# Optimization experiments

Hardware: AMD Instinct MI355X
Metric: run time of the kernel (lower is better)

## Reference

```python
import jax, jax.numpy as jnp
import numpy as np

N_NODES = 100000
N_EDGES = 1600000
D_FEAT = 64
D_OUT = 64


def setup_inputs() -> dict:
    key = jax.random.key(0)
    k1, k2, k3, k4 = jax.random.split(key, 4)
    vertices = jax.random.normal(k1, (N_NODES, D_FEAT), dtype=jnp.float32)
    edges = jax.random.randint(k2, (2, N_EDGES), 0, N_NODES, dtype=jnp.int64)
    weight = jax.random.normal(k3, (D_OUT, D_FEAT), dtype=jnp.float32) * (1.0 / np.sqrt(D_FEAT))
    bias = jax.random.normal(k4, (D_OUT,), dtype=jnp.float32) * 0.01
    return {"vertices": vertices, "edges": edges, "weight": weight, "bias": bias}


def reference(vertices, edges, weight, bias):
    # GraphConv forward, dense (non-sparse) path, self_loop=True, normalize=True.
    n_vertices = vertices.shape[0]
    idx = jnp.arange(n_vertices, dtype=edges.dtype)
    dst = jnp.concatenate([edges[0], idx])  # scatter destinations (edges[0])
    src = jnp.concatenate([edges[1], idx])  # gather sources (edges[1])
    # agg[i] = sum over edges with dst==i of vertices[src]
    agg = jax.ops.segment_sum(vertices[src], dst, num_segments=n_vertices)
    # degree per node (torch scatters ones_like(neighbours): all feature cols equal)
    deg = jax.ops.segment_sum(
        jnp.ones_like(dst, dtype=vertices.dtype), dst, num_segments=n_vertices
    )
    agg = agg * (jnp.clip(deg, 1.0, None) ** -0.5)[:, None]
    # Linear: y = agg @ W.T + b
    return agg @ weight.T + bias
```

## Files before the change

kernel.cpp:

```cpp
#include <hip/hip_runtime.h>
#include <hip/hip_fp16.h>

constexpr int N_NODES = 100000;
constexpr int N_EDGES = 1600000;
constexpr int D = 64;

constexpr int SHC    = 9;
constexpr int BSZC   = 1 << SHC;
constexpr int NBC    = (N_NODES + BSZC - 1) / BSZC;
constexpr int SPLITB = 256;
constexpr int TILE   = (N_EDGES + SPLITB - 1) / SPLITB;
constexpr int LINB   = 2048;
constexpr int TILE2  = 8192;
constexpr int NBLK2  = (N_EDGES + TILE2 - 1) / TILE2;

constexpr int SCAN_CHUNK = 1024;
constexpr int NCHUNK = (N_NODES + SCAN_CHUNK - 1) / SCAN_CHUNK;

__device__ __forceinline__ int waveInclScan(int v, int lane) {
    #pragma unroll
    for (int off = 1; off < 64; off <<= 1) {
        int t = __shfl_up(v, off, 64);
        if (lane >= off) v += t;
    }
    return v;
}

__global__ __launch_bounds__(256, 2) void lin_hist(
    const float* __restrict__ vertices,
    const float* __restrict__ weight,
    __half* __restrict__ Yh,
    const int* __restrict__ edges,
    int* __restrict__ bcntC)
{
    if (blockIdx.x < LINB) {
        __shared__ __align__(16) float rowbuf[8][64];
        const int wid  = threadIdx.x >> 6;
        const int lane = threadIdx.x & 63;

        float w[64];
        #pragma unroll
        for (int f = 0; f < 64; ++f) w[f] = weight[lane * 64 + f];

        const int nodesPerIter = LINB * 8;
        for (int base = blockIdx.x * 8; base < N_NODES; base += nodesPerIter) {
            const int n0 = base + wid * 2;
            const int n1 = n0 + 1;
            float a0 = 0.0f, a1 = 0.0f;
            if (n0 < N_NODES) a0 = vertices[(size_t)n0 * D + lane];
            if (n1 < N_NODES) a1 = vertices[(size_t)n1 * D + lane];
            rowbuf[wid * 2][lane]     = a0;
            rowbuf[wid * 2 + 1][lane] = a1;
            __syncthreads();
            float acc0 = 0.0f, acc1 = 0.0f;
            const float4* r0 = reinterpret_cast<const float4*>(&rowbuf[wid * 2][0]);
            const float4* r1 = reinterpret_cast<const float4*>(&rowbuf[wid * 2 + 1][0]);
            #pragma unroll
            for (int f4 = 0; f4 < 16; ++f4) {
                float4 q0 = r0[f4];
                float4 q1 = r1[f4];
                acc0 += q0.x * w[4*f4] + q0.y * w[4*f4+1] + q0.z * w[4*f4+2] + q0.w * w[4*f4+3];
                acc1 += q1.x * w[4*f4] + q1.y * w[4*f4+1] + q1.z * w[4*f4+2] + q1.w * w[4*f4+3];
            }
            if (n0 < N_NODES) Yh[(size_t)n0 * D + lane] = __float2half(acc0);
            if (n1 < N_NODES) Yh[(size_t)n1 * D + lane] = __float2half(acc1);
            __syncthreads();
        }
    } else {
        __shared__ int h[NBC];
        const int b = blockIdx.x - LINB;
        if (threadIdx.x < NBC) h[threadIdx.x] = 0;
        __syncthreads();
        const int lo = b * TILE;
        const int hi = min(lo + TILE, N_EDGES);
        for (int e = lo + threadIdx.x; e < hi; e += 256)
            atomicAdd(&h[edges[e] >> SHC], 1);
        __syncthreads();
        if (threadIdx.x < NBC) {
            int v = h[threadIdx.x];
            if (v) atomicAdd(&bcntC[threadIdx.x], v);
        }
    }
}

__global__ __launch_bounds__(1024) void s_scatter(const int* __restrict__ edges,
                                                  const int* __restrict__ bcntC,
                                                  int* __restrict__ cursorDelta,
                                                  int* __restrict__ bbaseC,
                                                  int* __restrict__ packed)
{
    __shared__ int s[256];
    __shared__ int baseC[NBC];
    __shared__ int h[NBC];
    __shared__ int chunk[NBC];
    const int t = threadIdx.x;

    int v = 0;
    if (t < 256) { v = (t < NBC) ? bcntC[t] : 0; s[t] = v; }
    __syncthreads();
    for (int o = 1; o < 256; o <<= 1) {
        int u = (t < 256 && t >= o) ? s[t - o] : 0;
        __syncthreads();
        if (t < 256) s[t] += u;
        __syncthreads();
    }
    if (t < NBC) {
        int e = s[t] - v;
        baseC[t] = e;
        h[t] = 0;
        if (blockIdx.x == 0) bbaseC[t] = e;
    }
    __syncthreads();

    const int lo = blockIdx.x * TILE2;
    int myd[8];
    #pragma unroll
    for (int k = 0; k < 8; ++k) {
        int e = lo + k * 1024 + t;
        myd[k] = (e < N_EDGES) ? edges[e] : -1;
        if (myd[k] >= 0) atomicAdd(&h[myd[k] >> SHC], 1);
    }
    __syncthreads();

    if (t < NBC) {
        int c = h[t];
        chunk[t] = c ? (baseC[t] + atomicAdd(&cursorDelta[t], c)) : 0;
        h[t] = 0;
    }
    __syncthreads();

    #pragma unroll
    for (int k = 0; k < 8; ++k) {
        if (myd[k] >= 0) {
            int e = lo + k * 1024 + t;
            int src = edges[N_EDGES + e];
            int j = myd[k] >> SHC;
            int r = atomicAdd(&h[j], 1);
            packed[chunk[j] + r] = (src << SHC) | (myd[k] & (BSZC - 1));
        }
    }
}

__global__ __launch_bounds__(1024) void csr512(const int* __restrict__ packed,
                                               const int* __restrict__ bbaseC,
                                               const int* __restrict__ bcntC,
                                               int* __restrict__ offsets,
                                               int* __restrict__ deg,
                                               int* __restrict__ srt)
{
    __shared__ int h2[BSZC];
    __shared__ int cur2[BSZC];
    __shared__ int s[BSZC];
    const int b = blockIdx.x;
    const int t = threadIdx.x;
    const int start = bbaseC[b];
    const int cnt   = bcntC[b];

    if (t < BSZC) h2[t] = 0;
    __syncthreads();

    int myp[8];
    #pragma unroll
    for (int k = 0; k < 8; ++k) {
        int i = k * 1024 + t;
        myp[k] = (i < cnt) ? packed[start + i] : -1;
        if (myp[k] >= 0) atomicAdd(&h2[myp[k] & (BSZC - 1)], 1);
    }
    for (int i = 8192 + t; i < cnt; i += 1024)
        atomicAdd(&h2[packed[start + i] & (BSZC - 1)], 1);
    __syncthreads();

    if (t < BSZC) s[t] = h2[t];
    __syncthreads();
    for (int o = 1; o < BSZC; o <<= 1) {
        int u = (t < BSZC && t >= o) ? s[t - o] : 0;
        __syncthreads();
        if (t < BSZC) s[t] += u;
        __syncthreads();
    }
    if (t < BSZC) {
        int excl = s[t] - h2[t];
        int node = (b << SHC) + t;
        if (node < N_NODES) { offsets[node] = start + excl; deg[node] = h2[t]; }
        cur2[t] = excl;
    }
    __syncthreads();

    #pragma unroll
    for (int k = 0; k < 8; ++k) {
        if (myp[k] >= 0) {
            int r = atomicAdd(&cur2[myp[k] & (BSZC - 1)], 1);
            srt[start + r] = myp[k] >> SHC;
        }
    }
    for (int i = 8192 + t; i < cnt; i += 1024) {
        int p = packed[start + i];
        int r = atomicAdd(&cur2[p & (BSZC - 1)], 1);
        srt[start + r] = p >> SHC;
    }
}

__device__ __forceinline__ void addrow(float* acc, uint4 u)
{
    const __half2* h = reinterpret_cast<const __half2*>(&u);
    #pragma unroll
    for (int k = 0; k < 4; ++k) {
        float2 f = __half22float2(h[k]);
        acc[2 * k]     += f.x;
        acc[2 * k + 1] += f.y;
    }
}

__global__ __launch_bounds__(256) void gather_h(
    const __half* __restrict__ Yh,
    const int* __restrict__ offsets,
    const int* __restrict__ deg,
    const int* __restrict__ srt,
    const float* __restrict__ bias,
    float* __restrict__ out)
{
    const int wid  = threadIdx.x >> 6;
    const int lane = threadIdx.x & 63;
    const int g    = lane >> 3;
    const int sub  = lane & 7;
    const int n0   = blockIdx.x * 8 + wid * 2;
    const int n1   = n0 + 1;
    if (n0 >= N_NODES) return;
    const bool has1 = (n1 < N_NODES);

    const int st0 = offsets[n0];
    const int c0  = deg[n0];
    int st1 = 0, c1 = 0;
    if (has1) { st1 = offsets[n1]; c1 = deg[n1]; }

    float a0[8], a1[8];
    #pragma unroll
    for (int j = 0; j < 8; ++j) { a0[j] = 0.0f; a1[j] = 0.0f; }

    if (g == 0) {
        uint4 u0 = *reinterpret_cast<const uint4*>(Yh + (size_t)n0 * D + sub * 8);
        addrow(a0, u0);
        if (has1) {
            uint4 u1 = *reinterpret_cast<const uint4*>(Yh + (size_t)n1 * D + sub * 8);
            addrow(a1, u1);
        }
    }

    const int m = min(c0 & ~7, c1 & ~7);
    int e = 0;
    for (; e < m; e += 8) {
        int s0 = srt[st0 + e + g];
        int s1 = srt[st1 + e + g];
        uint4 u0 = *reinterpret_cast<const uint4*>(Yh + (size_t)s0 * D + sub * 8);
        uint4 u1 = *reinterpret_cast<const uint4*>(Yh + (size_t)s1 * D + sub * 8);
        addrow(a0, u0);
        addrow(a1, u1);
    }

    int e0 = e;
    for (; e0 + 16 <= c0; e0 += 16) {
        int s0 = srt[st0 + e0 + g];
        int s1 = srt[st0 + e0 + 8 + g];
        uint4 u0 = *reinterpret_cast<const uint4*>(Yh + (size_t)s0 * D + sub * 8);
        uint4 u1 = *reinterpret_cast<const uint4*>(Yh + (size_t)s1 * D + sub * 8);
        addrow(a0, u0);
        addrow(a0, u1);
    }
    if (e0 + 8 <= c0) {
        int s0 = srt[st0 + e0 + g];
        uint4 u0 = *reinterpret_cast<const uint4*>(Yh + (size_t)s0 * D + sub * 8);
        addrow(a0, u0);
        e0 += 8;
    }
    if (e0 + g < c0) {
        int s0 = srt[st0 + e0 + g];
        uint4 u0 = *reinterpret_cast<const uint4*>(Yh + (size_t)s0 * D + sub * 8);
        addrow(a0, u0);
    }

    if (has1) {
        int e1 = e;
        for (; e1 + 16 <= c1; e1 += 16) {
            int s0 = srt[st1 + e1 + g];
            int s1 = srt[st1 + e1 + 8 + g];
            uint4 u0 = *reinterpret_cast<const uint4*>(Yh + (size_t)s0 * D + sub * 8);
            uint4 u1 = *reinterpret_cast<const uint4*>(Yh + (size_t)s1 * D + sub * 8);
            addrow(a1, u0);
            addrow(a1, u1);
        }
        if (e1 + 8 <= c1) {
            int s0 = srt[st1 + e1 + g];
            uint4 u0 = *reinterpret_cast<const uint4*>(Yh + (size_t)s0 * D + sub * 8);
            addrow(a1, u0);
            e1 += 8;
        }
        if (e1 + g < c1) {
            int s0 = srt[st1 + e1 + g];
            uint4 u0 = *reinterpret_cast<const uint4*>(Yh + (size_t)s0 * D + sub * 8);
            addrow(a1, u0);
        }
    }

    #pragma unroll
    for (int j = 0; j < 8; ++j) {
        a0[j] += __shfl_xor(a0[j], 8, 64);
        a0[j] += __shfl_xor(a0[j], 16, 64);
        a0[j] += __shfl_xor(a0[j], 32, 64);
        a1[j] += __shfl_xor(a1[j], 8, 64);
        a1[j] += __shfl_xor(a1[j], 16, 64);
        a1[j] += __shfl_xor(a1[j], 32, 64);
    }

    if (g == 0) {
        const float4 b0 = *reinterpret_cast<const float4*>(bias + sub * 8);
        const float4 b1 = *reinterpret_cast<const float4*>(bias + sub * 8 + 4);
        {
            const float sc = rsqrtf((float)c0 + 1.0f);
            float4 r0, r1;
            r0.x = a0[0] * sc + b0.x;  r0.y = a0[1] * sc + b0.y;
            r0.z = a0[2] * sc + b0.z;  r0.w = a0[3] * sc + b0.w;
            r1.x = a0[4] * sc + b1.x;  r1.y = a0[5] * sc + b1.y;
            r1.z = a0[6] * sc + b1.z;  r1.w = a0[7] * sc + b1.w;
            *reinterpret_cast<float4*>(out + (size_t)n0 * D + sub * 8)     = r0;
            *reinterpret_cast<float4*>(out + (size_t)n0 * D + sub * 8 + 4) = r1;
        }
        if (has1) {
            const float sc = rsqrtf((float)c1 + 1.0f);
            float4 r0, r1;
            r0.x = a1[0] * sc + b0.x;  r0.y = a1[1] * sc + b0.y;
            r0.z = a1[2] * sc + b0.z;  r0.w = a1[3] * sc + b0.w;
            r1.x = a1[4] * sc + b1.x;  r1.y = a1[5] * sc + b1.y;
            r1.z = a1[6] * sc + b1.z;  r1.w = a1[7] * sc + b1.w;
            *reinterpret_cast<float4*>(out + (size_t)n1 * D + sub * 8)     = r0;
            *reinterpret_cast<float4*>(out + (size_t)n1 * D + sub * 8 + 4) = r1;
        }
    }
}


__global__ __launch_bounds__(256) void linear_kernel(
    const float* __restrict__ vertices,
    const float* __restrict__ weight,
    float* __restrict__ Y)
{
    __shared__ float rowbuf[4][64];
    const int wid  = threadIdx.x >> 6;
    const int lane = threadIdx.x & 63;
    float w[64];
    #pragma unroll
    for (int f = 0; f < 64; ++f) w[f] = weight[lane * 64 + f];
    const int nodesPerIter = gridDim.x * 4;
    for (int base = blockIdx.x * 4; base < N_NODES; base += nodesPerIter) {
        const int node = base + wid;
        float a = 0.0f;
        if (node < N_NODES) a = vertices[(size_t)node * D + lane];
        rowbuf[wid][lane] = a;
        __syncthreads();
        float acc = 0.0f;
        #pragma unroll
        for (int f = 0; f < 64; ++f)
            acc += rowbuf[wid][f] * w[f];
        if (node < N_NODES) Y[(size_t)node * D + lane] = acc;
        __syncthreads();
    }
}

__global__ __launch_bounds__(256) void gather_f32(
    const float* __restrict__ Y,
    const int* __restrict__ offsets,
    const int* __restrict__ deg,
    const int* __restrict__ sortedSrc,
    const float* __restrict__ bias,
    float* __restrict__ out)
{
    const int wid  = threadIdx.x >> 6;
    const int lane = threadIdx.x & 63;
    const int g    = lane >> 4;
    const int sub  = lane & 15;
    const int node = blockIdx.x * 4 + wid;
    if (node >= N_NODES) return;

    const int start = offsets[node];
    const int cnt   = deg[node];

    float4 acc;
    if (g == 0) {
        acc = *reinterpret_cast<const float4*>(Y + (size_t)node * D + (sub << 2));
    } else {
        acc.x = 0.0f; acc.y = 0.0f; acc.z = 0.0f; acc.w = 0.0f;
    }

    int e = 0;
    for (; e + 8 <= cnt; e += 8) {
        int s0 = sortedSrc[start + e + g];
        int s1 = sortedSrc[start + e + 4 + g];
        const float4 a0 = *reinterpret_cast<const float4*>(Y + (size_t)s0 * D + (sub << 2));
        const float4 a1 = *reinterpret_cast<const float4*>(Y + (size_t)s1 * D + (sub << 2));
        acc.x += a0.x; acc.y += a0.y; acc.z += a0.z; acc.w += a0.w;
        acc.x += a1.x; acc.y += a1.y; acc.z += a1.z; acc.w += a1.w;
    }
    if (e + 4 <= cnt) {
        int s0 = sortedSrc[start + e + g];
        const float4 a0 = *reinterpret_cast<const float4*>(Y + (size_t)s0 * D + (sub << 2));
        acc.x += a0.x; acc.y += a0.y; acc.z += a0.z; acc.w += a0.w;
        e += 4;
    }
    if (e + g < cnt) {
        int s0 = sortedSrc[start + e + g];
        const float4 a0 = *reinterpret_cast<const float4*>(Y + (size_t)s0 * D + (sub << 2));
        acc.x += a0.x; acc.y += a0.y; acc.z += a0.z; acc.w += a0.w;
    }

    acc.x += __shfl_xor(acc.x, 16, 64);
    acc.y += __shfl_xor(acc.y, 16, 64);
    acc.z += __shfl_xor(acc.z, 16, 64);
    acc.w += __shfl_xor(acc.w, 16, 64);
    acc.x += __shfl_xor(acc.x, 32, 64);
    acc.y += __shfl_xor(acc.y, 32, 64);
    acc.z += __shfl_xor(acc.z, 32, 64);
    acc.w += __shfl_xor(acc.w, 32, 64);

    if (lane < 16) {
        const float sc = rsqrtf((float)cnt + 1.0f);
        const float4 b4 = *reinterpret_cast<const float4*>(bias + (sub << 2));
        float4 r;
        r.x = acc.x * sc + b4.x;
        r.y = acc.y * sc + b4.y;
        r.z = acc.z * sc + b4.z;
        r.w = acc.w * sc + b4.w;
        *reinterpret_cast<float4*>(out + (size_t)node * D + (sub << 2)) = r;
    }
}

__global__ __launch_bounds__(256) void hist_kernel(const int* __restrict__ edges,
                                                   int* __restrict__ deg)
{
    int e = blockIdx.x * 256 + threadIdx.x;
    if (e < N_EDGES) atomicAdd(&deg[edges[e]], 1);
}

__global__ __launch_bounds__(256) void scan_part(const int* __restrict__ deg,
                                                 int* __restrict__ partial)
{
    int t = threadIdx.x;
    int base = blockIdx.x * SCAN_CHUNK + t * 4;
    int s = 0;
    #pragma unroll
    for (int k = 0; k < 4; ++k) { int i = base + k; if (i < N_NODES) s += deg[i]; }
    int lane = t & 63, wid = t >> 6;
    #pragma unroll
    for (int off = 32; off; off >>= 1) s += __shfl_down(s, off, 64);
    __shared__ int red[4];
    if (lane == 0) red[wid] = s;
    __syncthreads();
    if (t == 0) partial[blockIdx.x] = red[0] + red[1] + red[2] + red[3];
}

__global__ void scan_small(int* partial) {
    int lane = threadIdx.x;
    int v0 = (lane < NCHUNK) ? partial[lane] : 0;
    int v1 = (64 + lane < NCHUNK) ? partial[64 + lane] : 0;
    int i0 = waveInclScan(v0, lane);
    int tot0 = __shfl(i0, 63, 64);
    int i1 = waveInclScan(v1, lane) + tot0;
    if (lane < NCHUNK) partial[lane] = i0 - v0;
    if (64 + lane < NCHUNK) partial[64 + lane] = i1 - v1;
}

__global__ __launch_bounds__(256) void scan_final(const int* __restrict__ deg,
                                                  const int* __restrict__ partial,
                                                  int* __restrict__ offsets,
                                                  int* __restrict__ cursor)
{
    int t = threadIdx.x;
    int base = blockIdx.x * SCAN_CHUNK + t * 4;
    int d[4]; int s = 0;
    #pragma unroll
    for (int k = 0; k < 4; ++k) { int i = base + k; d[k] = (i < N_NODES) ? deg[i] : 0; s += d[k]; }
    __shared__ int sd[256];
    sd[t] = s; __syncthreads();
    #pragma unroll
    for (int off = 1; off < 256; off <<= 1) {
        int v = (t >= off) ? sd[t - off] : 0;
        __syncthreads();
        sd[t] += v;
        __syncthreads();
    }
    int excl = sd[t] - s + partial[blockIdx.x];
    #pragma unroll
    for (int k = 0; k < 4; ++k) {
        int i = base + k;
        if (i < N_NODES) { offsets[i] = excl; cursor[i] = excl; excl += d[k]; }
    }
}

__global__ __launch_bounds__(256) void scatter_idx(const int* __restrict__ edges,
                                                   int* __restrict__ cursor,
                                                   int* __restrict__ sortedSrc)
{
    int e = blockIdx.x * 256 + threadIdx.x;
    if (e >= N_EDGES) return;
    int dst = edges[e];
    int src = edges[N_EDGES + e];
    int pos = atomicAdd(&cursor[dst], 1);
    sortedSrc[pos] = src;
}


__global__ __launch_bounds__(256) void fb_scatter(
    const float* __restrict__ vertices, const int* __restrict__ edges,
    float* __restrict__ agg, float* __restrict__ degF)
{
    long long tid = (long long)blockIdx.x * 256 + threadIdx.x;
    int lane = threadIdx.x & 63;
    long long e = tid >> 6;
    if (e >= N_EDGES) return;
    int dst = edges[e];
    int src = edges[N_EDGES + e];
    atomicAdd(&agg[(size_t)dst * D + lane], vertices[(size_t)src * D + lane]);
    if (lane == 0) atomicAdd(&degF[dst], 1.0f);
}

__global__ __launch_bounds__(256) void fb_finish(
    const float* __restrict__ vertices, const float* __restrict__ weight,
    const float* __restrict__ bias, const float* __restrict__ degF,
    float* __restrict__ out)
{
    __shared__ float rowbuf[4][64];
    const int wid  = threadIdx.x >> 6;
    const int lane = threadIdx.x & 63;
    float w[64];
    #pragma unroll
    for (int f = 0; f < 64; ++f) w[f] = weight[lane * 64 + f];
    const float b = bias[lane];
    const int nodesPerIter = gridDim.x * 4;
    for (int base = blockIdx.x * 4; base < N_NODES; base += nodesPerIter) {
        const int node = base + wid;
        float a = 0.0f;
        if (node < N_NODES) {
            const float scale = rsqrtf(degF[node] + 1.0f);
            a = (out[(size_t)node * D + lane] + vertices[(size_t)node * D + lane]) * scale;
        }
        rowbuf[wid][lane] = a;
        __syncthreads();
        float acc = b;
        #pragma unroll
        for (int f = 0; f < 64; ++f) acc += rowbuf[wid][f] * w[f];
        if (node < N_NODES) out[(size_t)node * D + lane] = acc;
        __syncthreads();
    }
}

extern "C" void kernel_launch(void* const* d_in, const int* in_sizes, int n_in,
                              void* d_out, int out_size, void* d_ws, size_t ws_size,
                              hipStream_t stream) {
    const float* vertices = (const float*)d_in[0];
    const int*   edges    = (const int*)d_in[1];
    const float* weight   = (const float*)d_in[2];
    const float* bias     = (const float*)d_in[3];
    float* out = (float*)d_out;

    const int threads = 256;
    const int edgeBlocks = (N_EDGES + threads - 1) / threads;

    {
        __half* Yh         = (__half*)d_ws;
        int*   bcntC       = (int*)(Yh + (size_t)N_NODES * D);
        int*   cursorDelta = bcntC + NBC;
        int*   bbaseC      = cursorDelta + NBC;
        int*   offs        = bbaseC + NBC;
        int*   deg         = offs + N_NODES;
        int*   packed      = deg + N_NODES;
        int*   srt         = packed + N_EDGES;
        size_t needed      = (size_t)((char*)(srt + N_EDGES) - (char*)d_ws);
        if (ws_size >= needed) {
            (void)hipMemsetAsync(bcntC, 0, sizeof(int) * 2 * NBC, stream);
            lin_hist<<<LINB + SPLITB, threads, 0, stream>>>(vertices, weight, Yh, edges, bcntC);
            s_scatter<<<NBLK2, 1024, 0, stream>>>(edges, bcntC, cursorDelta, bbaseC, packed);
            csr512<<<NBC, 1024, 0, stream>>>(packed, bbaseC, bcntC, offs, deg, srt);
            gather_h<<<(N_NODES + 7) / 8, threads, 0, stream>>>(Yh, offs, deg, srt, bias, out);
            return;
        }
    }

    {
        float* Y       = (float*)d_ws;
        int*   deg     = (int*)(Y + (size_t)N_NODES * D);
        int*   offs    = deg + N_NODES;
        int*   cursor  = offs + N_NODES;
        int*   partial = cursor + N_NODES;
        int*   srt     = partial + 128;
        size_t needed  = (size_t)((char*)(srt + N_EDGES) - (char*)d_ws);
        if (ws_size >= needed) {
            (void)hipMemsetAsync(deg, 0, sizeof(int) * N_NODES, stream);
            linear_kernel<<<1024, threads, 0, stream>>>(vertices, weight, Y);
            hist_kernel<<<edgeBlocks, threads, 0, stream>>>(edges, deg);
            scan_part<<<NCHUNK, threads, 0, stream>>>(deg, partial);
            scan_small<<<1, 64, 0, stream>>>(partial);
            scan_final<<<NCHUNK, threads, 0, stream>>>(deg, partial, offs, cursor);
            scatter_idx<<<edgeBlocks, threads, 0, stream>>>(edges, cursor, srt);
            gather_f32<<<(N_NODES + 3) / 4, threads, 0, stream>>>(Y, offs, deg, srt, bias, out);
            return;
        }
    }

    {
        float* degF = (float*)d_ws;
        (void)hipMemsetAsync(out, 0, sizeof(float) * (size_t)N_NODES * D, stream);
        (void)hipMemsetAsync(degF, 0, sizeof(float) * N_NODES, stream);
        const long long totalScatter = (long long)N_EDGES * 64;
        fb_scatter<<<(int)((totalScatter + threads - 1) / threads), threads, 0, stream>>>(
            vertices, edges, out, degF);
        fb_finish<<<1024, threads, 0, stream>>>(vertices, weight, bias, degF, out);
    }
}
```

Measured before the change: 113.4 us.

## Move linear transform after aggregation and fuse it into the gather kernel

The first kernel no longer computes the 64x64 linear transform. It only converts the vertex features to fp16, while the histogram work runs in the same launch as before. The gather kernel sums the raw fp16 features, normalises them, stages the result in shared memory, and applies the weight matrix and bias before writing the output. This removes a separate pass of matmul work and gives a lighter first-stage kernel. In exchange, every gather block reloads the weights, adds a block barrier, and rounds the inputs to fp16 before aggregation instead of rounding the transformed outputs.

```diff
diff --git a/kernel.cpp b/kernel.cpp
--- a/kernel.cpp
+++ b/kernel.cpp
@@ -10,7 +10,7 @@
 constexpr int NBC    = (N_NODES + BSZC - 1) / BSZC;
 constexpr int SPLITB = 256;
 constexpr int TILE   = (N_EDGES + SPLITB - 1) / SPLITB;
-constexpr int LINB   = 2048;
+constexpr int CVB    = 1024;
 constexpr int TILE2  = 8192;
 constexpr int NBLK2  = (N_EDGES + TILE2 - 1) / TILE2;
 
@@ -26,49 +26,32 @@
     return v;
 }
 
-__global__ __launch_bounds__(256, 2) void lin_hist(
+__global__ __launch_bounds__(256) void cvt_hist(
     const float* __restrict__ vertices,
-    const float* __restrict__ weight,
-    __half* __restrict__ Yh,
+    __half* __restrict__ Xh,
     const int* __restrict__ edges,
     int* __restrict__ bcntC)
 {
-    if (blockIdx.x < LINB) {
-        __shared__ __align__(16) float rowbuf[8][64];
-        const int wid  = threadIdx.x >> 6;
-        const int lane = threadIdx.x & 63;
-
-        float w[64];
-        #pragma unroll
-        for (int f = 0; f < 64; ++f) w[f] = weight[lane * 64 + f];
-
-        const int nodesPerIter = LINB * 8;
-        for (int base = blockIdx.x * 8; base < N_NODES; base += nodesPerIter) {
-            const int n0 = base + wid * 2;
-            const int n1 = n0 + 1;
-            float a0 = 0.0f, a1 = 0.0f;
-            if (n0 < N_NODES) a0 = vertices[(size_t)n0 * D + lane];
-            if (n1 < N_NODES) a1 = vertices[(size_t)n1 * D + lane];
-            rowbuf[wid * 2][lane]     = a0;
-            rowbuf[wid * 2 + 1][lane] = a1;
-            __syncthreads();
-            float acc0 = 0.0f, acc1 = 0.0f;
-            const float4* r0 = reinterpret_cast<const float4*>(&rowbuf[wid * 2][0]);
-            const float4* r1 = reinterpret_cast<const float4*>(&rowbuf[wid * 2 + 1][0]);
-            #pragma unroll
-            for (int f4 = 0; f4 < 16; ++f4) {
-                float4 q0 = r0[f4];
-                float4 q1 = r1[f4];
-                acc0 += q0.x * w[4*f4] + q0.y * w[4*f4+1] + q0.z * w[4*f4+2] + q0.w * w[4*f4+3];
-                acc1 += q1.x * w[4*f4] + q1.y * w[4*f4+1] + q1.z * w[4*f4+2] + q1.w * w[4*f4+3];
-            }
-            if (n0 < N_NODES) Yh[(size_t)n0 * D + lane] = __float2half(acc0);
-            if (n1 < N_NODES) Yh[(size_t)n1 * D + lane] = __float2half(acc1);
-            __syncthreads();
+    if (blockIdx.x < CVB) {
+        const int total8 = N_NODES * D / 8;
+        const float4* v4 = reinterpret_cast<const float4*>(vertices);
+        for (int i = blockIdx.x * 256 + threadIdx.x; i < total8; i += CVB * 256) {
+            float4 f0 = v4[2 * i];
+            float4 f1 = v4[2 * i + 1];
+            __half2 h01 = __floats2half2_rn(f0.x, f0.y);
+            __half2 h23 = __floats2half2_rn(f0.z, f0.w);
+            __half2 h45 = __floats2half2_rn(f1.x, f1.y);
+            __half2 h67 = __floats2half2_rn(f1.z, f1.w);
+            uint4 u;
+            u.x = *reinterpret_cast<const unsigned*>(&h01);
+            u.y = *reinterpret_cast<const unsigned*>(&h23);
+            u.z = *reinterpret_cast<const unsigned*>(&h45);
+            u.w = *reinterpret_cast<const unsigned*>(&h67);
+            *reinterpret_cast<uint4*>(Xh + (size_t)i * 8) = u;
         }
     } else {
         __shared__ int h[NBC];
-        const int b = blockIdx.x - LINB;
+        const int b = blockIdx.x - CVB;
         if (threadIdx.x < NBC) h[threadIdx.x] = 0;
         __syncthreads();
         const int lo = b * TILE;
@@ -211,14 +194,17 @@
     }
 }
 
-__global__ __launch_bounds__(256) void gather_h(
-    const __half* __restrict__ Yh,
+__global__ __launch_bounds__(256, 2) void gather_lin(
+    const __half* __restrict__ Xh,
     const int* __restrict__ offsets,
     const int* __restrict__ deg,
     const int* __restrict__ srt,
+    const float* __restrict__ weight,
     const float* __restrict__ bias,
     float* __restrict__ out)
 {
+    __shared__ __align__(16) float aggbuf[8][64];
+
     const int wid  = threadIdx.x >> 6;
     const int lane = threadIdx.x & 63;
     const int g    = lane >> 3;
@@ -238,10 +224,10 @@
     for (int j = 0; j < 8; ++j) { a0[j] = 0.0f; a1[j] = 0.0f; }
 
     if (g == 0) {
-        uint4 u0 = *reinterpret_cast<const uint4*>(Yh + (size_t)n0 * D + sub * 8);
+        uint4 u0 = *reinterpret_cast<const uint4*>(Xh + (size_t)n0 * D + sub * 8);
         addrow(a0, u0);
         if (has1) {
-            uint4 u1 = *reinterpret_cast<const uint4*>(Yh + (size_t)n1 * D + sub * 8);
+            uint4 u1 = *reinterpret_cast<const uint4*>(Xh + (size_t)n1 * D + sub * 8);
             addrow(a1, u1);
         }
     }
@@ -251,8 +237,8 @@
     for (; e < m; e += 8) {
         int s0 = srt[st0 + e + g];
         int s1 = srt[st1 + e + g];
-        uint4 u0 = *reinterpret_cast<const uint4*>(Yh + (size_t)s0 * D + sub * 8);
-        uint4 u1 = *reinterpret_cast<const uint4*>(Yh + (size_t)s1 * D + sub * 8);
+        uint4 u0 = *reinterpret_cast<const uint4*>(Xh + (size_t)s0 * D + sub * 8);
+        uint4 u1 = *reinterpret_cast<const uint4*>(Xh + (size_t)s1 * D + sub * 8);
         addrow(a0, u0);
         addrow(a1, u1);
     }
@@ -261,20 +247,20 @@
     for (; e0 + 16 <= c0; e0 += 16) {
         int s0 = srt[st0 + e0 + g];
         int s1 = srt[st0 + e0 + 8 + g];
-        uint4 u0 = *reinterpret_cast<const uint4*>(Yh + (size_t)s0 * D + sub * 8);
-        uint4 u1 = *reinterpret_cast<const uint4*>(Yh + (size_t)s1 * D + sub * 8);
+        uint4 u0 = *reinterpret_cast<const uint4*>(Xh + (size_t)s0 * D + sub * 8);
+        uint4 u1 = *reinterpret_cast<const uint4*>(Xh + (size_t)s1 * D + sub * 8);
         addrow(a0, u0);
         addrow(a0, u1);
     }
     if (e0 + 8 <= c0) {
         int s0 = srt[st0 + e0 + g];
-        uint4 u0 = *reinterpret_cast<const uint4*>(Yh + (size_t)s0 * D + sub * 8);
+        uint4 u0 = *reinterpret_cast<const uint4*>(Xh + (size_t)s0 * D + sub * 8);
         addrow(a0, u0);
         e0 += 8;
     }
     if (e0 + g < c0) {
         int s0 = srt[st0 + e0 + g];
-        uint4 u0 = *reinterpret_cast<const uint4*>(Yh + (size_t)s0 * D + sub * 8);
+        uint4 u0 = *reinterpret_cast<const uint4*>(Xh + (size_t)s0 * D + sub * 8);
         addrow(a0, u0);
     }
 
@@ -283,20 +269,20 @@
         for (; e1 + 16 <= c1; e1 += 16) {
             int s0 = srt[st1 + e1 + g];
             int s1 = srt[st1 + e1 + 8 + g];
-            uint4 u0 = *reinterpret_cast<const uint4*>(Yh + (size_t)s0 * D + sub * 8);
-            uint4 u1 = *reinterpret_cast<const uint4*>(Yh + (size_t)s1 * D + sub * 8);
+            uint4 u0 = *reinterpret_cast<const uint4*>(Xh + (size_t)s0 * D + sub * 8);
+            uint4 u1 = *reinterpret_cast<const uint4*>(Xh + (size_t)s1 * D + sub * 8);
             addrow(a1, u0);
             addrow(a1, u1);
         }
         if (e1 + 8 <= c1) {
             int s0 = srt[st1 + e1 + g];
-            uint4 u0 = *reinterpret_cast<const uint4*>(Yh + (size_t)s0 * D + sub * 8);
+            uint4 u0 = *reinterpret_cast<const uint4*>(Xh + (size_t)s0 * D + sub * 8);
             addrow(a1, u0);
             e1 += 8;
         }
         if (e1 + g < c1) {
             int s0 = srt[st1 + e1 + g];
-            uint4 u0 = *reinterpret_cast<const uint4*>(Yh + (size_t)s0 * D + sub * 8);
+            uint4 u0 = *reinterpret_cast<const uint4*>(Xh + (size_t)s0 * D + sub * 8);
             addrow(a1, u0);
         }
     }
@@ -312,29 +298,43 @@
     }
 
     if (g == 0) {
-        const float4 b0 = *reinterpret_cast<const float4*>(bias + sub * 8);
-        const float4 b1 = *reinterpret_cast<const float4*>(bias + sub * 8 + 4);
         {
             const float sc = rsqrtf((float)c0 + 1.0f);
-            float4 r0, r1;
-            r0.x = a0[0] * sc + b0.x;  r0.y = a0[1] * sc + b0.y;
-            r0.z = a0[2] * sc + b0.z;  r0.w = a0[3] * sc + b0.w;
-            r1.x = a0[4] * sc + b1.x;  r1.y = a0[5] * sc + b1.y;
-            r1.z = a0[6] * sc + b1.z;  r1.w = a0[7] * sc + b1.w;
-            *reinterpret_cast<float4*>(out + (size_t)n0 * D + sub * 8)     = r0;
-            *reinterpret_cast<float4*>(out + (size_t)n0 * D + sub * 8 + 4) = r1;
+            float4 q0, q1;
+            q0.x = a0[0] * sc; q0.y = a0[1] * sc; q0.z = a0[2] * sc; q0.w = a0[3] * sc;
+            q1.x = a0[4] * sc; q1.y = a0[5] * sc; q1.z = a0[6] * sc; q1.w = a0[7] * sc;
+            *reinterpret_cast<float4*>(&aggbuf[wid * 2][sub * 8])     = q0;
+            *reinterpret_cast<float4*>(&aggbuf[wid * 2][sub * 8 + 4]) = q1;
         }
         if (has1) {
             const float sc = rsqrtf((float)c1 + 1.0f);
-            float4 r0, r1;
-            r0.x = a1[0] * sc + b0.x;  r0.y = a1[1] * sc + b0.y;
-            r0.z = a1[2] * sc + b0.z;  r0.w = a1[3] * sc + b0.w;
-            r1.x = a1[4] * sc + b1.x;  r1.y = a1[5] * sc + b1.y;
-            r1.z = a1[6] * sc + b1.z;  r1.w = a1[7] * sc + b1.w;
-            *reinterpret_cast<float4*>(out + (size_t)n1 * D + sub * 8)     = r0;
-            *reinterpret_cast<float4*>(out + (size_t)n1 * D + sub * 8 + 4) = r1;
-        }
-    }
+            float4 q0, q1;
+            q0.x = a1[0] * sc; q0.y = a1[1] * sc; q0.z = a1[2] * sc; q0.w = a1[3] * sc;
+            q1.x = a1[4] * sc; q1.y = a1[5] * sc; q1.z = a1[6] * sc; q1.w = a1[7] * sc;
+            *reinterpret_cast<float4*>(&aggbuf[wid * 2 + 1][sub * 8])     = q0;
+            *reinterpret_cast<float4*>(&aggbuf[wid * 2 + 1][sub * 8 + 4]) = q1;
+        }
+    }
+    __syncthreads();
+
+    float4 w4[16];
+    const float4* wrow = reinterpret_cast<const float4*>(weight + (size_t)lane * 64);
+    #pragma unroll
+    for (int f4 = 0; f4 < 16; ++f4) w4[f4] = wrow[f4];
+    const float b = bias[lane];
+
+    const float4* r0 = reinterpret_cast<const float4*>(&aggbuf[wid * 2][0]);
+    const float4* r1 = reinterpret_cast<const float4*>(&aggbuf[wid * 2 + 1][0]);
+    float y0 = 0.0f, y1 = 0.0f;
+    #pragma unroll
+    for (int f4 = 0; f4 < 16; ++f4) {
+        float4 q0 = r0[f4];
+        float4 q1 = r1[f4];
+        y0 += q0.x * w4[f4].x + q0.y * w4[f4].y + q0.z * w4[f4].z + q0.w * w4[f4].w;
+        y1 += q1.x * w4[f4].x + q1.y * w4[f4].y + q1.z * w4[f4].z + q1.w * w4[f4].w;
+    }
+    out[(size_t)n0 * D + lane] = y0 + b;
+    if (has1) out[(size_t)n1 * D + lane] = y1 + b;
 }
 
 
@@ -564,8 +564,8 @@
     const int edgeBlocks = (N_EDGES + threads - 1) / threads;
 
     {
-        __half* Yh         = (__half*)d_ws;
-        int*   bcntC       = (int*)(Yh + (size_t)N_NODES * D);
+        __half* Xh         = (__half*)d_ws;
+        int*   bcntC       = (int*)(Xh + (size_t)N_NODES * D);
         int*   cursorDelta = bcntC + NBC;
         int*   bbaseC      = cursorDelta + NBC;
         int*   offs        = bbaseC + NBC;
@@ -575,10 +575,10 @@
         size_t needed      = (size_t)((char*)(srt + N_EDGES) - (char*)d_ws);
         if (ws_size >= needed) {
             (void)hipMemsetAsync(bcntC, 0, sizeof(int) * 2 * NBC, stream);
-            lin_hist<<<LINB + SPLITB, threads, 0, stream>>>(vertices, weight, Yh, edges, bcntC);
+            cvt_hist<<<CVB + SPLITB, threads, 0, stream>>>(vertices, Xh, edges, bcntC);
             s_scatter<<<NBLK2, 1024, 0, stream>>>(edges, bcntC, cursorDelta, bbaseC, packed);
             csr512<<<NBC, 1024, 0, stream>>>(packed, bbaseC, bcntC, offs, deg, srt);
-            gather_h<<<(N_NODES + 7) / 8, threads, 0, stream>>>(Yh, offs, deg, srt, bias, out);
+            gather_lin<<<(N_NODES + 7) / 8, threads, 0, stream>>>(Xh, offs, deg, srt, weight, bias, out);
             return;
         }
     }
```

After: 198.6 us. 75.1% more time.
